# Kernel optimization log

Measured on AMD Instinct MI355X. Metric: run time of the kernel, lower is better.

Reference implementation:

```python
import jax, jax.numpy as jnp
import numpy as np

B, N, H, HID, P = 4, 1024, 16, 64, 2


def setup_inputs() -> dict:
    key = jax.random.key(0)
    ks = jax.random.split(key, 8)
    positions = jax.random.normal(ks[0], (B, N, P), dtype=jnp.float32)
    key_padding_mask = jax.random.bernoulli(ks[1], 0.1, (B, N))
    # MLP params (Linear stores weight as (out,in) in torch; we keep (in,out) and matmul)
    s1 = 1.0 / np.sqrt(P)
    s2 = 1.0 / np.sqrt(HID)
    W1 = jax.random.uniform(ks[2], (P, HID), jnp.float32, -s1, s1)
    b1 = jax.random.uniform(ks[3], (HID,), jnp.float32, -s1, s1)
    W2 = jax.random.uniform(ks[4], (HID, HID), jnp.float32, -s2, s2)
    b2 = jax.random.uniform(ks[5], (HID,), jnp.float32, -s2, s2)
    W3 = jax.random.uniform(ks[6], (HID, H), jnp.float32, -s2, s2)
    b3 = jax.random.uniform(ks[7], (H,), jnp.float32, -s2, s2)
    return {"positions": positions, "key_padding_mask": key_padding_mask,
            "W1": W1, "b1": b1, "W2": W2, "b2": b2, "W3": W3, "b3": b3}


def reference(positions, key_padding_mask, W1, b1, W2, b2, W3, b3):
    # rel_pos[b, i, j] = pos[b, j] - pos[b, i]  -> (B, N, N, 2)
    rel = positions[:, None, :, :] - positions[:, :, None, :]
    h = jax.nn.relu(rel @ W1 + b1)          # (B, N, N, HID)
    h = jax.nn.relu(h @ W2 + b2)            # (B, N, N, HID)
    bias = h @ W3 + b3                      # (B, N, N, H)
    bias = jnp.transpose(bias, (0, 3, 1, 2))  # (B, H, N, N)
    # zero out rows/cols touching padded tokens
    combined = key_padding_mask[:, None, None, :] | key_padding_mask[:, None, :, None]
    bias = jnp.where(combined, 0.0, bias)
    return bias
```

## Files before the change

### kernel.cpp

```cpp
#include <hip/hip_runtime.h>
#include <hip/hip_bf16.h>
#include <hip/hip_fp16.h>

#define B_   4
#define N_   1024
#define H_   16
#define HID_ 64
#define TI   32
#define TJ   64
#define USJ  36

typedef float    f32x4  __attribute__((ext_vector_type(4)));
typedef __fp16   fp16x2 __attribute__((ext_vector_type(2)));
typedef _Float16 f16x8  __attribute__((ext_vector_type(8)));
typedef unsigned int u32;

union F16x8U { u32 u[4]; f16x8 v; };

static __device__ __forceinline__ u32 pk(float a, float b) {
    union { fp16x2 f; u32 u; } r;
    r.f = __builtin_amdgcn_cvt_pkrtz(a, b);
    return r.u;
}
static __device__ __forceinline__ u32 pkadd_relu(u32 a, u32 b) {
    union { u32 u; fp16x2 f; } x, y, r;
    x.u = a; y.u = b;
    fp16x2 z = { (__fp16)0.f, (__fp16)0.f };
    fp16x2 s = x.f + y.f;
    r.f = __builtin_elementwise_max(s, z);
    return r.u;
}
static __device__ __forceinline__ u32 pkcvt_relu(float a, float b) {
    union { fp16x2 f; u32 u; } r;
    fp16x2 z = { (__fp16)0.f, (__fp16)0.f };
    fp16x2 s = __builtin_amdgcn_cvt_pkrtz(a, b);
    r.f = __builtin_elementwise_max(s, z);
    return r.u;
}

__global__ __launch_bounds__(256) void RelativePositionalBias_kernel(
    const float* __restrict__ pos,
    const int*   __restrict__ mask,
    const float* __restrict__ W1,
    const float* __restrict__ b1,
    const float* __restrict__ W2,
    const float* __restrict__ b2,
    const float* __restrict__ W3,
    const float* __restrict__ b3,
    float* __restrict__ out)
{
    __shared__ __align__(16) u32 ujL[TJ][USJ];
    __shared__ __align__(16) u32 uinL[TI][USJ];

    const int b  = blockIdx.z;
    const int i0 = blockIdx.y * TI;
    const int j0 = blockIdx.x * TJ;
    const int tid = threadIdx.x;
    const int w = tid >> 6;
    const int l = tid & 63;
    const int g = l >> 4;
    const int c = l & 15;

    for (int it = tid; it < (TJ + TI) * 8; it += 256) {
        int r  = it >> 3;
        int qq = (it & 7) * 4;
        int k0 = qq * 2;
        int tok = (r < TJ) ? (j0 + r) : (i0 + (r - TJ));
        float2 p  = *(const float2*)&pos[(b * N_ + tok) * 2];
        float4 a0 = *(const float4*)&W1[k0];
        float4 a1 = *(const float4*)&W1[k0 + 4];
        float4 c0 = *(const float4*)&W1[HID_ + k0];
        float4 c1 = *(const float4*)&W1[HID_ + k0 + 4];
        float u0 = p.x*a0.x + p.y*c0.x, u1 = p.x*a0.y + p.y*c0.y;
        float u2 = p.x*a0.z + p.y*c0.z, u3 = p.x*a0.w + p.y*c0.w;
        float u4 = p.x*a1.x + p.y*c1.x, u5 = p.x*a1.y + p.y*c1.y;
        float u6 = p.x*a1.z + p.y*c1.z, u7 = p.x*a1.w + p.y*c1.w;
        uint4 o;
        if (r < TJ) {
            o.x = pk(u0, u1); o.y = pk(u2, u3); o.z = pk(u4, u5); o.w = pk(u6, u7);
            *(uint4*)&ujL[r][qq] = o;
        } else {
            float4 ba = *(const float4*)&b1[k0];
            float4 bb = *(const float4*)&b1[k0 + 4];
            o.x = pk(ba.x - u0, ba.y - u1); o.y = pk(ba.z - u2, ba.w - u3);
            o.z = pk(bb.x - u4, bb.y - u5); o.w = pk(bb.z - u6, bb.w - u7);
            *(uint4*)&uinL[r - TJ][qq] = o;
        }
    }

    F16x8U W2f[2][4];
    #pragma unroll
    for (int s = 0; s < 2; ++s)
        #pragma unroll
        for (int n = 0; n < 4; ++n)
            #pragma unroll
            for (int e = 0; e < 8; ++e)
                W2f[s][n].v[e] = (_Float16)W2[(32*s + 8*g + e) * HID_ + 16*n + c];

    F16x8U W3g[2];
    #pragma unroll
    for (int s = 0; s < 2; ++s)
        #pragma unroll
        for (int e = 0; e < 8; ++e)
            W3g[s].v[e] = (_Float16)W3[(32*s + 16*(e>>2) + 4*g + (e&3)) * H_ + c];

    f32x4 b2v[4];
    #pragma unroll
    for (int n = 0; n < 4; ++n)
        b2v[n] = *(const f32x4*)&b2[16*n + 4*g];

    const float b3v = b3[c];
    const int* maskb = &mask[b * N_ + i0];
    const int4 mj = *(const int4*)&mask[b * N_ + j0 + 16*w + 4*g];
    float* const outRow = out + ((size_t)(b*H_ + c) << 20) + (size_t)(j0 + 16*w + 4*g)
                              + ((size_t)i0 << 10);

    __syncthreads();

    const uint4 pj0 = *(const uint4*)&ujL[16*w + c][4*g];
    const uint4 pj1 = *(const uint4*)&ujL[16*w + c][16 + 4*g];

    #pragma unroll 4
    for (int t = 0; t < TI; ++t) {
        const int mi = maskb[t];
        f32x4 o = { 0.f, 0.f, 0.f, 0.f };

        if (!mi) {
            uint4 uiA = *(const uint4*)&uinL[t][4*g];
            uint4 uiB = *(const uint4*)&uinL[t][16 + 4*g];

            F16x8U A1[2];
            A1[0].u[0] = pkadd_relu(pj0.x, uiA.x);
            A1[0].u[1] = pkadd_relu(pj0.y, uiA.y);
            A1[0].u[2] = pkadd_relu(pj0.z, uiA.z);
            A1[0].u[3] = pkadd_relu(pj0.w, uiA.w);
            A1[1].u[0] = pkadd_relu(pj1.x, uiB.x);
            A1[1].u[1] = pkadd_relu(pj1.y, uiB.y);
            A1[1].u[2] = pkadd_relu(pj1.z, uiB.z);
            A1[1].u[3] = pkadd_relu(pj1.w, uiB.w);

            f32x4 acc[4];
            #pragma unroll
            for (int n = 0; n < 4; ++n) {
                acc[n] = __builtin_amdgcn_mfma_f32_16x16x32_f16(W2f[0][n].v, A1[0].v, b2v[n], 0, 0, 0);
                acc[n] = __builtin_amdgcn_mfma_f32_16x16x32_f16(W2f[1][n].v, A1[1].v, acc[n], 0, 0, 0);
            }

            F16x8U A3[2];
            #pragma unroll
            for (int s = 0; s < 2; ++s) {
                A3[s].u[0] = pkcvt_relu(acc[2*s][0],     acc[2*s][1]);
                A3[s].u[1] = pkcvt_relu(acc[2*s][2],     acc[2*s][3]);
                A3[s].u[2] = pkcvt_relu(acc[2*s + 1][0], acc[2*s + 1][1]);
                A3[s].u[3] = pkcvt_relu(acc[2*s + 1][2], acc[2*s + 1][3]);
            }

            f32x4 acc3 = { b3v, b3v, b3v, b3v };
            acc3 = __builtin_amdgcn_mfma_f32_16x16x32_f16(A3[0].v, W3g[0].v, acc3, 0, 0, 0);
            acc3 = __builtin_amdgcn_mfma_f32_16x16x32_f16(A3[1].v, W3g[1].v, acc3, 0, 0, 0);

            o[0] = mj.x ? 0.f : acc3[0];
            o[1] = mj.y ? 0.f : acc3[1];
            o[2] = mj.z ? 0.f : acc3[2];
            o[3] = mj.w ? 0.f : acc3[3];
        }

        *(f32x4*)(outRow + ((size_t)t << 10)) = o;
    }
}

extern "C" void kernel_launch(void* const* d_in, const int* in_sizes, int n_in,
                              void* d_out, int out_size, void* d_ws, size_t ws_size,
                              hipStream_t stream) {
    const float* pos  = (const float*)d_in[0];
    const int*   mask = (const int*)d_in[1];
    const float* W1   = (const float*)d_in[2];
    const float* b1   = (const float*)d_in[3];
    const float* W2   = (const float*)d_in[4];
    const float* b2   = (const float*)d_in[5];
    const float* W3   = (const float*)d_in[6];
    const float* b3   = (const float*)d_in[7];
    float* out = (float*)d_out;

    dim3 grid(N_ / TJ, N_ / TI, B_);
    RelativePositionalBias_kernel<<<grid, dim3(256), 0, stream>>>(
        pos, mask, W1, b1, W2, b2, W3, b3, out);
}
```

Measured before the change: 62.22 us.

## Assign one query row per wave, computing layer-1 in registers without LDS

```diff
diff --git a/kernel.cpp b/kernel.cpp
--- a/kernel.cpp
+++ b/kernel.cpp
@@ -6,9 +6,6 @@
 #define N_   1024
 #define H_   16
 #define HID_ 64
-#define TI   32
-#define TJ   64
-#define USJ  36
 
 typedef float    f32x4  __attribute__((ext_vector_type(4)));
 typedef __fp16   fp16x2 __attribute__((ext_vector_type(2)));
@@ -16,23 +13,18 @@
 typedef unsigned int u32;
 
 union F16x8U { u32 u[4]; f16x8 v; };
+union H2U    { fp16x2 f; u32 u; };
 
-static __device__ __forceinline__ u32 pk(float a, float b) {
-    union { fp16x2 f; u32 u; } r;
-    r.f = __builtin_amdgcn_cvt_pkrtz(a, b);
-    return r.u;
+static __device__ __forceinline__ fp16x2 pkb(float x) {
+    return __builtin_amdgcn_cvt_pkrtz(x, x);
 }
-static __device__ __forceinline__ u32 pkadd_relu(u32 a, u32 b) {
-    union { u32 u; fp16x2 f; } x, y, r;
-    x.u = a; y.u = b;
-    fp16x2 z = { (__fp16)0.f, (__fp16)0.f };
-    fp16x2 s = x.f + y.f;
-    r.f = __builtin_elementwise_max(s, z);
+static __device__ __forceinline__ u32 hmax0(fp16x2 a) {
+    H2U r; fp16x2 z = { (__fp16)0.f, (__fp16)0.f };
+    r.f = __builtin_elementwise_max(a, z);
     return r.u;
 }
 static __device__ __forceinline__ u32 pkcvt_relu(float a, float b) {
-    union { fp16x2 f; u32 u; } r;
-    fp16x2 z = { (__fp16)0.f, (__fp16)0.f };
+    H2U r; fp16x2 z = { (__fp16)0.f, (__fp16)0.f };
     fp16x2 s = __builtin_amdgcn_cvt_pkrtz(a, b);
     r.f = __builtin_elementwise_max(s, z);
     return r.u;
@@ -49,44 +41,23 @@
     const float* __restrict__ b3,
     float* __restrict__ out)
 {
-    __shared__ __align__(16) u32 ujL[TJ][USJ];
-    __shared__ __align__(16) u32 uinL[TI][USJ];
-
-    const int b  = blockIdx.z;
-    const int i0 = blockIdx.y * TI;
-    const int j0 = blockIdx.x * TJ;
+    const int b   = blockIdx.y;
     const int tid = threadIdx.x;
     const int w = tid >> 6;
     const int l = tid & 63;
     const int g = l >> 4;
     const int c = l & 15;
+    const int irow = blockIdx.x * 4 + w;
 
-    for (int it = tid; it < (TJ + TI) * 8; it += 256) {
-        int r  = it >> 3;
-        int qq = (it & 7) * 4;
-        int k0 = qq * 2;
-        int tok = (r < TJ) ? (j0 + r) : (i0 + (r - TJ));
-        float2 p  = *(const float2*)&pos[(b * N_ + tok) * 2];
-        float4 a0 = *(const float4*)&W1[k0];
-        float4 a1 = *(const float4*)&W1[k0 + 4];
-        float4 c0 = *(const float4*)&W1[HID_ + k0];
-        float4 c1 = *(const float4*)&W1[HID_ + k0 + 4];
-        float u0 = p.x*a0.x + p.y*c0.x, u1 = p.x*a0.y + p.y*c0.y;
-        float u2 = p.x*a0.z + p.y*c0.z, u3 = p.x*a0.w + p.y*c0.w;
-        float u4 = p.x*a1.x + p.y*c1.x, u5 = p.x*a1.y + p.y*c1.y;
-        float u6 = p.x*a1.z + p.y*c1.z, u7 = p.x*a1.w + p.y*c1.w;
-        uint4 o;
-        if (r < TJ) {
-            o.x = pk(u0, u1); o.y = pk(u2, u3); o.z = pk(u4, u5); o.w = pk(u6, u7);
-            *(uint4*)&ujL[r][qq] = o;
-        } else {
-            float4 ba = *(const float4*)&b1[k0];
-            float4 bb = *(const float4*)&b1[k0 + 4];
-            o.x = pk(ba.x - u0, ba.y - u1); o.y = pk(ba.z - u2, ba.w - u3);
-            o.z = pk(bb.x - u4, bb.y - u5); o.w = pk(bb.z - u6, bb.w - u7);
-            *(uint4*)&uinL[r - TJ][qq] = o;
+    fp16x2 w1a[2][4], w1b[2][4], uin[2][4];
+    #pragma unroll
+    for (int s = 0; s < 2; ++s)
+        #pragma unroll
+        for (int e2 = 0; e2 < 4; ++e2) {
+            int k = 32*s + 8*g + 2*e2;
+            w1a[s][e2] = __builtin_amdgcn_cvt_pkrtz(W1[k],        W1[k+1]);
+            w1b[s][e2] = __builtin_amdgcn_cvt_pkrtz(W1[HID_ + k], W1[HID_ + k + 1]);
         }
-    }
 
     F16x8U W2f[2][4];
     #pragma unroll
@@ -108,64 +79,71 @@
     #pragma unroll
     for (int n = 0; n < 4; ++n)
         b2v[n] = *(const f32x4*)&b2[16*n + 4*g];
+    const float b3v = b3[c];
 
-    const float b3v = b3[c];
-    const int* maskb = &mask[b * N_ + i0];
-    const int4 mj = *(const int4*)&mask[b * N_ + j0 + 16*w + 4*g];
-    float* const outRow = out + ((size_t)(b*H_ + c) << 20) + (size_t)(j0 + 16*w + 4*g)
-                              + ((size_t)i0 << 10);
+    {
+        float2 pi = *(const float2*)&pos[(b * N_ + irow) * 2];
+        fp16x2 nx = pkb(-pi.x), ny = pkb(-pi.y);
+        #pragma unroll
+        for (int s = 0; s < 2; ++s)
+            #pragma unroll
+            for (int e2 = 0; e2 < 4; ++e2) {
+                int k = 32*s + 8*g + 2*e2;
+                fp16x2 b1p = __builtin_amdgcn_cvt_pkrtz(b1[k], b1[k+1]);
+                uin[s][e2] = nx * w1a[s][e2] + (ny * w1b[s][e2] + b1p);
+            }
+    }
 
-    __syncthreads();
+    const int mi = mask[b * N_ + irow];
+    const float2* pos2  = (const float2*)pos + (size_t)b * N_;
+    const int*    maskj = mask + (size_t)b * N_;
+    float* const outRow = out + ((size_t)(b*H_ + c) << 20) + ((size_t)irow << 10) + 4*g;
 
-    const uint4 pj0 = *(const uint4*)&ujL[16*w + c][4*g];
-    const uint4 pj1 = *(const uint4*)&ujL[16*w + c][16 + 4*g];
+    if (mi) {
+        const f32x4 z = { 0.f, 0.f, 0.f, 0.f };
+        for (int jb = 0; jb < N_; jb += 16)
+            *(f32x4*)(outRow + jb) = z;
+        return;
+    }
 
-    #pragma unroll 4
-    for (int t = 0; t < TI; ++t) {
-        const int mi = maskb[t];
-        f32x4 o = { 0.f, 0.f, 0.f, 0.f };
+    for (int jb = 0; jb < N_; jb += 16) {
+        float2 pj = pos2[jb + c];
+        fp16x2 px = pkb(pj.x), py = pkb(pj.y);
 
-        if (!mi) {
-            uint4 uiA = *(const uint4*)&uinL[t][4*g];
-            uint4 uiB = *(const uint4*)&uinL[t][16 + 4*g];
+        F16x8U A1[2];
+        #pragma unroll
+        for (int s = 0; s < 2; ++s)
+            #pragma unroll
+            for (int e2 = 0; e2 < 4; ++e2)
+                A1[s].u[e2] = hmax0(px * w1a[s][e2] + (py * w1b[s][e2] + uin[s][e2]));
 
-            F16x8U A1[2];
-            A1[0].u[0] = pkadd_relu(pj0.x, uiA.x);
-            A1[0].u[1] = pkadd_relu(pj0.y, uiA.y);
-            A1[0].u[2] = pkadd_relu(pj0.z, uiA.z);
-            A1[0].u[3] = pkadd_relu(pj0.w, uiA.w);
-            A1[1].u[0] = pkadd_relu(pj1.x, uiB.x);
-            A1[1].u[1] = pkadd_relu(pj1.y, uiB.y);
-            A1[1].u[2] = pkadd_relu(pj1.z, uiB.z);
-            A1[1].u[3] = pkadd_relu(pj1.w, uiB.w);
-
-            f32x4 acc[4];
-            #pragma unroll
-            for (int n = 0; n < 4; ++n) {
-                acc[n] = __builtin_amdgcn_mfma_f32_16x16x32_f16(W2f[0][n].v, A1[0].v, b2v[n], 0, 0, 0);
-                acc[n] = __builtin_amdgcn_mfma_f32_16x16x32_f16(W2f[1][n].v, A1[1].v, acc[n], 0, 0, 0);
-            }
-
-            F16x8U A3[2];
-            #pragma unroll
-            for (int s = 0; s < 2; ++s) {
-                A3[s].u[0] = pkcvt_relu(acc[2*s][0],     acc[2*s][1]);
-                A3[s].u[1] = pkcvt_relu(acc[2*s][2],     acc[2*s][3]);
-                A3[s].u[2] = pkcvt_relu(acc[2*s + 1][0], acc[2*s + 1][1]);
-                A3[s].u[3] = pkcvt_relu(acc[2*s + 1][2], acc[2*s + 1][3]);
-            }
-
-            f32x4 acc3 = { b3v, b3v, b3v, b3v };
-            acc3 = __builtin_amdgcn_mfma_f32_16x16x32_f16(A3[0].v, W3g[0].v, acc3, 0, 0, 0);
-            acc3 = __builtin_amdgcn_mfma_f32_16x16x32_f16(A3[1].v, W3g[1].v, acc3, 0, 0, 0);
-
-            o[0] = mj.x ? 0.f : acc3[0];
-            o[1] = mj.y ? 0.f : acc3[1];
-            o[2] = mj.z ? 0.f : acc3[2];
-            o[3] = mj.w ? 0.f : acc3[3];
+        f32x4 acc[4];
+        #pragma unroll
+        for (int n = 0; n < 4; ++n) {
+            acc[n] = __builtin_amdgcn_mfma_f32_16x16x32_f16(W2f[0][n].v, A1[0].v, b2v[n], 0, 0, 0);
+            acc[n] = __builtin_amdgcn_mfma_f32_16x16x32_f16(W2f[1][n].v, A1[1].v, acc[n], 0, 0, 0);
         }
 
-        *(f32x4*)(outRow + ((size_t)t << 10)) = o;
+        F16x8U A3[2];
+        #pragma unroll
+        for (int s = 0; s < 2; ++s) {
+            A3[s].u[0] = pkcvt_relu(acc[2*s][0],     acc[2*s][1]);
+            A3[s].u[1] = pkcvt_relu(acc[2*s][2],     acc[2*s][3]);
+            A3[s].u[2] = pkcvt_relu(acc[2*s + 1][0], acc[2*s + 1][1]);
+            A3[s].u[3] = pkcvt_relu(acc[2*s + 1][2], acc[2*s + 1][3]);
+        }
+
+        f32x4 acc3 = { b3v, b3v, b3v, b3v };
+        acc3 = __builtin_amdgcn_mfma_f32_16x16x32_f16(A3[0].v, W3g[0].v, acc3, 0, 0, 0);
+        acc3 = __builtin_amdgcn_mfma_f32_16x16x32_f16(A3[1].v, W3g[1].v, acc3, 0, 0, 0);
+
+        const int4 mj = *(const int4*)&maskj[jb + 4*g];
+        f32x4 o;
+        o[0] = mj.x ? 0.f : acc3[0];
+        o[1] = mj.y ? 0.f : acc3[1];
+        o[2] = mj.z ? 0.f : acc3[2];
+        o[3] = mj.w ? 0.f : acc3[3];
+        *(f32x4*)(outRow + jb) = o;
     }
 }
 
@@ -182,7 +160,7 @@
     const float* b3   = (const float*)d_in[7];
     float* out = (float*)d_out;
 
-    dim3 grid(N_ / TJ, N_ / TI, B_);
+    dim3 grid(N_ / 4, B_);
     RelativePositionalBias_kernel<<<grid, dim3(256), 0, stream>>>(
         pos, mask, W1, b1, W2, b2, W3, b3, out);
 }
```

Measured after the change: 82.41 us. 32.4% more time.
